# Optimization experiments

Measured on AMD Instinct MI355X. Metric: run time of the kernel, lower is better.

The kernel has to match this reference:

```python
import jax, jax.numpy as jnp
import numpy as np

N = 50000      # num nodes
E = 800000     # num edges (avg degree 16)
H = 128        # hidden_dim
D = 3          # node_dim (decoder output)
L = 4          # num_layers


def setup_inputs() -> dict:
    key = jax.random.key(0)
    ks = jax.random.split(key, 6)
    s = 0.05
    x = jax.random.normal(ks[0], (N, H), dtype=jnp.float32)
    edge_index = jax.random.randint(ks[1], (2, E), 0, N, dtype=jnp.int64)
    # per-layer EdgeConv MLP params: Linear(2H->H), ReLU, Linear(H->H)
    W1 = jax.random.normal(ks[2], (L, 2 * H, H), dtype=jnp.float32) * s
    b1 = jnp.zeros((L, H), dtype=jnp.float32)
    W2 = jax.random.normal(ks[3], (L, H, H), dtype=jnp.float32) * s
    b2 = jnp.zeros((L, H), dtype=jnp.float32)
    # final fc: Linear(H -> D)
    Wf = jax.random.normal(ks[4], (H, D), dtype=jnp.float32) * s
    bf = jnp.zeros((D,), dtype=jnp.float32)
    return {"x": x, "edge_index": edge_index, "W1": W1, "b1": b1,
            "W2": W2, "b2": b2, "Wf": Wf, "bf": bf}


def reference(x, edge_index, W1, b1, W2, b2, Wf, bf):
    n = x.shape[0]
    # add_self_loops: every node has at least one incoming message
    loops = jnp.arange(n, dtype=edge_index.dtype)
    src = jnp.concatenate([edge_index[0], loops])  # x_j source
    dst = jnp.concatenate([edge_index[1], loops])  # x_i target / aggregate index
    for l in range(W1.shape[0]):
        x_i = x[dst]                                   # [E+N, H] gather targets
        x_j = x[src]                                   # [E+N, H] gather sources
        msg = jnp.concatenate([x_i, x_j - x_i], axis=-1)   # [E+N, 2H]
        msg = jax.nn.relu(msg @ W1[l] + b1[l]) @ W2[l] + b2[l]  # edge MLP
        x = jax.ops.segment_max(msg, dst, num_segments=n)       # max aggregate
    return x @ Wf + bf  # [N, D]
```

## Files before the change

### kernel.cpp

```cpp
#include <hip/hip_runtime.h>
#include <hip/hip_fp16.h>

typedef _Float16 f16;
typedef _Float16 f16x8 __attribute__((ext_vector_type(8)));
typedef __fp16 hf16x2 __attribute__((ext_vector_type(2)));
typedef float f32x4 __attribute__((ext_vector_type(4)));
typedef float f32x2 __attribute__((ext_vector_type(2)));

#define HDIM 128
#define LAYERS 4
#define NEG_BIG (-3.0e38f)

static __device__ __forceinline__ f32x4 mfma16(f16x8 a, f16x8 b, f32x4 c) {
  return __builtin_amdgcn_mfma_f32_16x16x32_f16(a, b, c, 0, 0, 0);
}

static __device__ __forceinline__ void atomicMaxF(float* addr, float val) {
  if (val >= 0.f) atomicMax((int*)addr, __float_as_int(val));
  else            atomicMin((unsigned int*)addr, __float_as_uint(val));
}

static __device__ __forceinline__ void split8(f32x4 a, f32x4 b, f16x8& hv, f16x8& lv) {
  hf16x2 h0 = __builtin_amdgcn_cvt_pkrtz(a.x, a.y);
  hf16x2 h1 = __builtin_amdgcn_cvt_pkrtz(a.z, a.w);
  hf16x2 h2 = __builtin_amdgcn_cvt_pkrtz(b.x, b.y);
  hf16x2 h3 = __builtin_amdgcn_cvt_pkrtz(b.z, b.w);
  hv[0]=(f16)h0[0]; hv[1]=(f16)h0[1]; hv[2]=(f16)h1[0]; hv[3]=(f16)h1[1];
  hv[4]=(f16)h2[0]; hv[5]=(f16)h2[1]; hv[6]=(f16)h3[0]; hv[7]=(f16)h3[1];
  hf16x2 l0 = __builtin_amdgcn_cvt_pkrtz(a.x-(float)h0[0], a.y-(float)h0[1]);
  hf16x2 l1 = __builtin_amdgcn_cvt_pkrtz(a.z-(float)h1[0], a.w-(float)h1[1]);
  hf16x2 l2 = __builtin_amdgcn_cvt_pkrtz(b.x-(float)h2[0], b.y-(float)h2[1]);
  hf16x2 l3 = __builtin_amdgcn_cvt_pkrtz(b.z-(float)h3[0], b.w-(float)h3[1]);
  lv[0]=(f16)l0[0]; lv[1]=(f16)l0[1]; lv[2]=(f16)l1[0]; lv[3]=(f16)l1[1];
  lv[4]=(f16)l2[0]; lv[5]=(f16)l2[1]; lv[6]=(f16)l3[0]; lv[7]=(f16)l3[1];
}

__global__ void gnn_hist(const int* __restrict__ ei, int* __restrict__ deg, int E) {
  int e = blockIdx.x * 256 + threadIdx.x;
  if (e < E) atomicAdd(&deg[ei[E + e]], 1);
}

__global__ void gnn_bsum(const int* __restrict__ deg, int* __restrict__ bsum, int N) {
  __shared__ int red[256];
  int v = blockIdx.x * 256 + threadIdx.x;
  red[threadIdx.x] = (v < N) ? (deg[v] + 1) : 0;
  __syncthreads();
  for (int d = 128; d; d >>= 1) {
    if (threadIdx.x < d) red[threadIdx.x] += red[threadIdx.x + d];
    __syncthreads();
  }
  if (threadIdx.x == 0) bsum[blockIdx.x] = red[0];
}

__global__ void gnn_bscan(const int* __restrict__ bsum, int* __restrict__ boffs,
                          int* __restrict__ offs, int nb, int N) {
  __shared__ int sh[256];
  int t = threadIdx.x;
  sh[t] = (t < nb) ? bsum[t] : 0;
  __syncthreads();
  for (int d = 1; d < 256; d <<= 1) {
    int add = (t >= d) ? sh[t - d] : 0;
    __syncthreads();
    sh[t] += add;
    __syncthreads();
  }
  boffs[t] = (t > 0) ? sh[t - 1] : 0;
  if (t == 255) offs[N] = sh[255];
}

__global__ void gnn_scan_fin(const int* __restrict__ deg, const int* __restrict__ boffs,
                             int* __restrict__ offs, int* __restrict__ cursor,
                             int* __restrict__ colsrc, int* __restrict__ nodeof, int N) {
  __shared__ int sh[256];
  int t = threadIdx.x;
  int v = blockIdx.x * 256 + t;
  int val = (v < N) ? (deg[v] + 1) : 0;
  sh[t] = val;
  __syncthreads();
  for (int d = 1; d < 256; d <<= 1) {
    int add = (t >= d) ? sh[t - d] : 0;
    __syncthreads();
    sh[t] += add;
    __syncthreads();
  }
  if (v < N) {
    int excl = boffs[blockIdx.x] + sh[t] - val;
    offs[v] = excl;
    cursor[v] = excl + 1;
    colsrc[excl] = v;
    int e = excl + val;
    for (int s = excl; s < e; s++) nodeof[s] = v;
  }
}

__global__ void gnn_scatter(const int* __restrict__ ei, int* __restrict__ cursor,
                            int* __restrict__ colsrc, int E) {
  int e = blockIdx.x * 256 + threadIdx.x;
  if (e < E) {
    int d = ei[E + e];
    int p = atomicAdd(&cursor[d], 1);
    colsrc[p] = ei[e];
  }
}

__global__ void gnn_biasprep(const float* __restrict__ W1, const float* __restrict__ b1,
                             const float* __restrict__ b2, const float* __restrict__ Wf,
                             const float* __restrict__ bf, float* __restrict__ cbias,
                             float* __restrict__ bfp) {
  int l = blockIdx.x, c = threadIdx.x;
  if (l < LAYERS) {
    float s = 0.f;
    if (l > 0) {
      const float* bp = b2 + (size_t)(l - 1) * HDIM;
      if (c < 128) {
        for (int k = 0; k < 128; k++)
          s += bp[k] * (W1[((size_t)l * 256 + k) * 128 + c] - W1[((size_t)l * 256 + 128 + k) * 128 + c]);
      } else {
        int cc = c - 128;
        for (int k = 0; k < 128; k++)
          s += bp[k] * W1[((size_t)l * 256 + 128 + k) * 128 + cc];
      }
    }
    float base = (c < 128) ? b1[(size_t)l * HDIM + c] : 0.f;
    cbias[l * 256 + c] = base + s;
  } else if (c < 3) {
    float s = bf[c];
    for (int k = 0; k < 128; k++) s += b2[3 * HDIM + k] * Wf[k * 3 + c];
    bfp[c] = s;
  }
}

__global__ void gnn_wprep1(const float* __restrict__ W1, f16* __restrict__ Wc) {
  int id = blockIdx.x * 256 + threadIdx.x;
  if (id >= LAYERS * 128 * 256) return;
  int col = id & 255, k = (id >> 8) & 127, l = id >> 15;
  float w;
  if (col < 128) w = W1[((size_t)l * 256 + k) * 128 + col] - W1[((size_t)l * 256 + 128 + k) * 128 + col];
  else           w = W1[((size_t)l * 256 + 128 + k) * 128 + (col - 128)];
  f16 hi = (f16)w;
  f16 lo = (f16)(w - (float)hi);
  int kk = k >> 5, quad = (k >> 3) & 3, j = k & 7;
  int ntile = col >> 4, lane = quad * 16 + (col & 15);
  size_t base = ((((size_t)l * 2 + 0) * 4 + kk) * 16 + ntile) * 512 + lane * 8 + j;
  Wc[base] = hi;
  Wc[base + (size_t)4 * 16 * 512] = lo;
}

__global__ void gnn_wprep2(const float* __restrict__ W2, f16* __restrict__ W2f) {
  int id = blockIdx.x * 256 + threadIdx.x;
  if (id >= LAYERS * 128 * 128) return;
  int n = id & 127, k = (id >> 7) & 127, l = id >> 14;
  float w = W2[((size_t)l * 128 + k) * 128 + n];
  f16 hi = (f16)w;
  f16 lo = (f16)(w - (float)hi);
  int kk = k >> 5, quad = (k >> 3) & 3, j = k & 7;
  int ntile = n >> 4, lane = quad * 16 + (n & 15);
  size_t base = ((((size_t)l * 2 + 0) * 4 + kk) * 8 + ntile) * 512 + lane * 8 + j;
  W2f[base] = hi;
  W2f[base + (size_t)4 * 8 * 512] = lo;
}

__global__ __launch_bounds__(256) void gnn_pq(const float* __restrict__ x,
    const f16* __restrict__ Wc, const float* __restrict__ cbias,
    float* __restrict__ P, float* __restrict__ Q, int N,
    const int* __restrict__ offs, int spb, float* __restrict__ xinit) {
  __shared__ __align__(16) f16 shA[2 * 4 * 4 * 64 * 8];
  int tid = threadIdx.x;
  int row0 = blockIdx.x * 64;
#pragma unroll
  for (int i = 0; i < 4; i++) {
    int p = i * 256 + tid;
    int row = p & 63, seg = p >> 6;
    f32x4 a = {}, b = {};
    int gr = row0 + row;
    if (gr < N) {
      const f32x4* xp = (const f32x4*)(x + (size_t)gr * HDIM + seg * 8);
      a = xp[0]; b = xp[1];
    }
    f16x8 hv, lv;
    split8(a, b, hv, lv);
    int kk = seg >> 2, quad = seg & 3, mt = row >> 4, m = row & 15;
    int lane = quad * 16 + m;
    int off = ((kk * 4 + mt) * 64 + lane) * 8;
    *(f16x8*)&shA[off] = hv;
    *(f16x8*)&shA[off + 4 * 4 * 64 * 8] = lv;
  }
  __syncthreads();
  int wave = tid >> 6, lane = tid & 63;
  int quad = lane >> 4, cl = lane & 15;
  f16x8 bw[2][4][4];
#pragma unroll
  for (int pl = 0; pl < 2; pl++)
#pragma unroll
    for (int nt = 0; nt < 4; nt++)
#pragma unroll
      for (int kk = 0; kk < 4; kk++) {
        int ntile = wave * 4 + nt;
        bw[pl][nt][kk] = *(const f16x8*)&Wc[(((size_t)(pl * 4 + kk) * 16 + ntile) * 64 + lane) * 8];
      }
#pragma unroll
  for (int mt = 0; mt < 4; mt++) {
    f32x4 acc[4] = {};
#pragma unroll
    for (int kk = 0; kk < 4; kk++) {
      f16x8 ah = *(const f16x8*)&shA[((kk * 4 + mt) * 64 + lane) * 8];
      f16x8 al = *(const f16x8*)&shA[(((4 + kk) * 4 + mt) * 64 + lane) * 8];
#pragma unroll
      for (int nt = 0; nt < 4; nt++) {
        acc[nt] = mfma16(ah, bw[0][nt][kk], acc[nt]);
        acc[nt] = mfma16(al, bw[0][nt][kk], acc[nt]);
        acc[nt] = mfma16(ah, bw[1][nt][kk], acc[nt]);
      }
    }
#pragma unroll
    for (int nt = 0; nt < 4; nt++) {
      int c = (wave * 4 + nt) * 16 + cl;
      float bb = cbias[c];
      float* dst = (c < HDIM) ? P : Q;
      int cc = c & 127;
#pragma unroll
      for (int i = 0; i < 4; i++) {
        int gr = row0 + mt * 16 + quad * 4 + i;
        if (gr < N) dst[(size_t)gr * HDIM + cc] = acc[nt][i] + bb;
      }
    }
  }
  if (tid < 64) {
    int v = row0 + tid;
    if (v < N) {
      int a = offs[v], b = offs[v + 1] - 1;
      if (a / spb != b / spb) {
        f32x4 ninf = {NEG_BIG, NEG_BIG, NEG_BIG, NEG_BIG};
        float* xr = xinit + (size_t)v * HDIM;
#pragma unroll
        for (int c = 0; c < HDIM; c += 4) *(f32x4*)(xr + c) = ninf;
      }
    }
  }
}

__global__ __launch_bounds__(256, 3) void gnn_edge3(
    const float* __restrict__ P, const float* __restrict__ Q,
    const int* __restrict__ offs, const int* __restrict__ colsrc,
    const int* __restrict__ nodeof, const f16* __restrict__ W2f,
    float* __restrict__ xout, int S, int spb) {
  __shared__ __align__(16) f16 shA[2 * 4 * 2 * 64 * 8];
  __shared__ float msg[32 * 132];
  __shared__ float stradV[2][128];
  __shared__ int stradN[2];
  int tid = threadIdx.x;
  int wave = tid >> 6, lane = tid & 63;
  int quad = lane >> 4, cl = lane & 15;
  f16x8 bw[2][2][4];
#pragma unroll
  for (int pl = 0; pl < 2; pl++)
#pragma unroll
    for (int nt = 0; nt < 2; nt++)
#pragma unroll
      for (int kk = 0; kk < 4; kk++)
        bw[pl][nt][kk] = *(const f16x8*)&W2f[(((size_t)(pl * 4 + kk) * 8 + (wave * 2 + nt)) * 64 + lane) * 8];
  int blk0 = blockIdx.x * spb;
  int blk1 = blk0 + spb; if (blk1 > S) blk1 = S;
  if (tid < 2) stradN[tid] = -1;
  int sl = tid >> 4, seg = tid & 15;
  int kkb = seg >> 2, qb = seg & 3;
  int laneF = qb * 16 + sl;
  int tc = 0;
  for (int t0 = blk0; t0 < blk1; t0 += 32, tc++) {
    int par = tc & 1, prv = par ^ 1;
    int tEnd = t0 + 32; if (tEnd > blk1) tEnd = blk1;
#pragma unroll
    for (int i = 0; i < 2; i++) {
      int slot = t0 + i * 16 + sl;
      int slc = (slot < S) ? slot : (S - 1);
      int src = colsrc[slc];
      int dst = nodeof[slc];
      const f32x4* qp = (const f32x4*)(Q + (size_t)src * HDIM + seg * 8);
      const f32x4* pp = (const f32x4*)(P + (size_t)dst * HDIM + seg * 8);
      f32x4 qa = qp[0], qb4 = qp[1], pa = pp[0], pb = pp[1];
      f32x4 sa, sb;
      sa.x = fmaxf(pa.x + qa.x, 0.f); sa.y = fmaxf(pa.y + qa.y, 0.f);
      sa.z = fmaxf(pa.z + qa.z, 0.f); sa.w = fmaxf(pa.w + qa.w, 0.f);
      sb.x = fmaxf(pb.x + qb4.x, 0.f); sb.y = fmaxf(pb.y + qb4.y, 0.f);
      sb.z = fmaxf(pb.z + qb4.z, 0.f); sb.w = fmaxf(pb.w + qb4.w, 0.f);
      f16x8 hv, lv;
      split8(sa, sb, hv, lv);
      int off = ((kkb * 2 + i) * 64 + laneF) * 8;
      *(f16x8*)&shA[off] = hv;
      *(f16x8*)&shA[off + 4096] = lv;
    }
    __syncthreads();
    if (tid == 0) stradN[par] = -1;
    f32x4 acc[2][2] = {};
#pragma unroll
    for (int kk = 0; kk < 4; kk++)
#pragma unroll
      for (int mt = 0; mt < 2; mt++) {
        int off = ((kk * 2 + mt) * 64 + lane) * 8;
        f16x8 ah = *(const f16x8*)&shA[off];
        f16x8 al = *(const f16x8*)&shA[off + 4096];
#pragma unroll
        for (int nt = 0; nt < 2; nt++) {
          acc[mt][nt] = mfma16(ah, bw[0][nt][kk], acc[mt][nt]);
          acc[mt][nt] = mfma16(al, bw[0][nt][kk], acc[mt][nt]);
          acc[mt][nt] = mfma16(ah, bw[1][nt][kk], acc[mt][nt]);
        }
      }
#pragma unroll
    for (int mt = 0; mt < 2; mt++)
#pragma unroll
      for (int nt = 0; nt < 2; nt++) {
        int col = wave * 32 + nt * 16 + cl;
#pragma unroll
        for (int i = 0; i < 4; i++) {
          int row = mt * 16 + quad * 4 + i;
          msg[row * 132 + col] = acc[mt][nt][i];
        }
      }
    __syncthreads();
    int vA = nodeof[t0];
    int vB = nodeof[tEnd - 1];
    int sNp = stradN[prv];
    int npairs = (vB - vA + 1) << 7;
    for (int p = tid; p < npairs; p += 256) {
      int v = vA + (p >> 7), col = p & 127;
      int a = offs[v], b = offs[v + 1];
      int r0 = (a > t0 ? a : t0) - t0;
      int r1 = (b < tEnd ? b : tEnd) - t0;
      float m = NEG_BIG;
      for (int r = r0; r < r1; r++) m = fmaxf(m, msg[r * 132 + col]);
      if (v == sNp) m = fmaxf(m, stradV[prv][col]);
      if (b > tEnd && tEnd < blk1) {
        stradV[par][col] = m;
        if (col == 0) stradN[par] = v;
      } else {
        float* dp = &xout[(size_t)v * HDIM + col];
        if (a < blk0 || b > blk1) atomicMaxF(dp, m);
        else *dp = m;
      }
    }
  }
}

__global__ __launch_bounds__(256) void gnn_fc(const float* __restrict__ x,
    const float* __restrict__ Wf, const float* __restrict__ bfp,
    float* __restrict__ out, int N) {
  int wave = threadIdx.x >> 6, lane = threadIdx.x & 63;
  int wid = blockIdx.x * 4 + wave, nw = gridDim.x * 4;
  int k0 = lane * 2;
  float w00 = Wf[k0 * 3 + 0], w01 = Wf[k0 * 3 + 1], w02 = Wf[k0 * 3 + 2];
  float w10 = Wf[k0 * 3 + 3], w11 = Wf[k0 * 3 + 4], w12 = Wf[k0 * 3 + 5];
  float bf0 = bfp[0], bf1 = bfp[1], bf2 = bfp[2];
  for (int v = wid; v < N; v += nw) {
    f32x2 xx = *(const f32x2*)(x + (size_t)v * HDIM + k0);
    float d0 = xx.x * w00 + xx.y * w10;
    float d1 = xx.x * w01 + xx.y * w11;
    float d2 = xx.x * w02 + xx.y * w12;
#pragma unroll
    for (int s = 32; s; s >>= 1) {
      d0 += __shfl_xor(d0, s, 64);
      d1 += __shfl_xor(d1, s, 64);
      d2 += __shfl_xor(d2, s, 64);
    }
    if (lane == 0) {
      out[(size_t)v * 3 + 0] = d0 + bf0;
      out[(size_t)v * 3 + 1] = d1 + bf1;
      out[(size_t)v * 3 + 2] = d2 + bf2;
    }
  }
}

extern "C" void kernel_launch(void* const* d_in, const int* in_sizes, int n_in,
                              void* d_out, int out_size, void* d_ws, size_t ws_size,
                              hipStream_t stream) {
  const float* x_in = (const float*)d_in[0];
  const int*   ei   = (const int*)d_in[1];
  const float* W1   = (const float*)d_in[2];
  const float* b1   = (const float*)d_in[3];
  const float* W2   = (const float*)d_in[4];
  const float* b2   = (const float*)d_in[5];
  const float* Wf   = (const float*)d_in[6];
  const float* bfv  = (const float*)d_in[7];
  float* outp = (float*)d_out;
  int N = in_sizes[0] / HDIM;
  int E = in_sizes[1] / 2;
  int S = E + N;

  char* ws = (char*)d_ws;
  size_t o = 0;
  auto alloc = [&](size_t bytes) -> char* {
    char* p = ws + o;
    o += (bytes + 255) & ~(size_t)255;
    return p;
  };
  int*   deg    = (int*)alloc((size_t)N * 4);
  int*   offs   = (int*)alloc(((size_t)N + 1) * 4);
  int*   cursor = (int*)alloc((size_t)N * 4);
  int*   colsrc = (int*)alloc((size_t)S * 4);
  int*   nodeof = (int*)alloc((size_t)S * 4);
  int*   bsum   = (int*)alloc(256 * 4);
  int*   boffs  = (int*)alloc(256 * 4);
  float* cbias  = (float*)alloc((size_t)LAYERS * 256 * 4);
  float* bfp    = (float*)alloc(4 * 4);
  float* P      = (float*)alloc((size_t)N * HDIM * 4);
  float* Q      = (float*)alloc((size_t)N * HDIM * 4);
  float* xbuf   = (float*)alloc((size_t)N * HDIM * 4);
  f16*   Wc     = (f16*)alloc((size_t)LAYERS * 65536 * 2);
  f16*   W2f    = (f16*)alloc((size_t)LAYERS * 32768 * 2);
  (void)ws_size; (void)n_in; (void)out_size;

  int nb = (N + 255) / 256;
  hipMemsetAsync(deg, 0, (size_t)N * 4, stream);
  gnn_hist<<<(E + 255) / 256, 256, 0, stream>>>(ei, deg, E);
  gnn_bsum<<<nb, 256, 0, stream>>>(deg, bsum, N);
  gnn_bscan<<<1, 256, 0, stream>>>(bsum, boffs, offs, nb, N);
  gnn_scan_fin<<<nb, 256, 0, stream>>>(deg, boffs, offs, cursor, colsrc, nodeof, N);
  gnn_scatter<<<(E + 255) / 256, 256, 0, stream>>>(ei, cursor, colsrc, E);
  gnn_biasprep<<<LAYERS + 1, 256, 0, stream>>>(W1, b1, b2, Wf, bfv, cbias, bfp);
  gnn_wprep1<<<(LAYERS * 128 * 256 + 255) / 256, 256, 0, stream>>>(W1, Wc);
  gnn_wprep2<<<(LAYERS * 128 * 128 + 255) / 256, 256, 0, stream>>>(W2, W2f);

  int spb = (((S + 1023) / 1024) + 31) & ~31;
  int NB = (S + spb - 1) / spb;
  const float* xc = x_in;
  for (int l = 0; l < LAYERS; l++) {
    gnn_pq<<<(N + 63) / 64, 256, 0, stream>>>(xc, Wc + (size_t)l * 65536, cbias + l * 256,
                                              P, Q, N, offs, spb, xbuf);
    gnn_edge3<<<NB, 256, 0, stream>>>(P, Q, offs, colsrc, nodeof, W2f + (size_t)l * 32768,
                                      xbuf, S, spb);
    xc = xbuf;
  }
  gnn_fc<<<256, 256, 0, stream>>>(xc, Wf, bfp, outp, N);
}
```

Measured before the change: 867.5 us.

## Enlarge edge tile to 48 rows and vectorize segment-max reduction

Raises the edge tile in the fused edge MLP kernel from 32 to 48 slots, so each barrier and weight-register pass covers more MFMA work, and aligns the per-block slot span to the new tile size. The segment-max reduction now has each thread handle four columns with f32x4 shared-memory loads and vector global stores instead of one column per thread. The f16 hi/lo split packs converted pairs via bitcast instead of element-wise assignment. The larger tile raises shared-memory use and accumulator registers, which may lower occupancy under the 3-blocks launch bound.

After: 926.7 us. 6.8% more time.

```diff
diff --git a/kernel.cpp b/kernel.cpp
--- a/kernel.cpp
+++ b/kernel.cpp
@@ -6,9 +6,12 @@
 typedef __fp16 hf16x2 __attribute__((ext_vector_type(2)));
 typedef float f32x4 __attribute__((ext_vector_type(4)));
 typedef float f32x2 __attribute__((ext_vector_type(2)));
+typedef unsigned int u32;
+typedef u32 u32x4 __attribute__((ext_vector_type(4)));
 
 #define HDIM 128
 #define LAYERS 4
+#define TS 48
 #define NEG_BIG (-3.0e38f)
 
 static __device__ __forceinline__ f32x4 mfma16(f16x8 a, f16x8 b, f32x4 c) {
@@ -18,6 +21,12 @@
 static __device__ __forceinline__ void atomicMaxF(float* addr, float val) {
   if (val >= 0.f) atomicMax((int*)addr, __float_as_int(val));
   else            atomicMin((unsigned int*)addr, __float_as_uint(val));
+}
+
+static __device__ __forceinline__ f16x8 pack4(hf16x2 a, hf16x2 b, hf16x2 c, hf16x2 d) {
+  u32x4 u = {__builtin_bit_cast(u32, a), __builtin_bit_cast(u32, b),
+             __builtin_bit_cast(u32, c), __builtin_bit_cast(u32, d)};
+  return __builtin_bit_cast(f16x8, u);
 }
 
 static __device__ __forceinline__ void split8(f32x4 a, f32x4 b, f16x8& hv, f16x8& lv) {
@@ -25,14 +34,12 @@
   hf16x2 h1 = __builtin_amdgcn_cvt_pkrtz(a.z, a.w);
   hf16x2 h2 = __builtin_amdgcn_cvt_pkrtz(b.x, b.y);
   hf16x2 h3 = __builtin_amdgcn_cvt_pkrtz(b.z, b.w);
-  hv[0]=(f16)h0[0]; hv[1]=(f16)h0[1]; hv[2]=(f16)h1[0]; hv[3]=(f16)h1[1];
-  hv[4]=(f16)h2[0]; hv[5]=(f16)h2[1]; hv[6]=(f16)h3[0]; hv[7]=(f16)h3[1];
-  hf16x2 l0 = __builtin_amdgcn_cvt_pkrtz(a.x-(float)h0[0], a.y-(float)h0[1]);
-  hf16x2 l1 = __builtin_amdgcn_cvt_pkrtz(a.z-(float)h1[0], a.w-(float)h1[1]);
-  hf16x2 l2 = __builtin_amdgcn_cvt_pkrtz(b.x-(float)h2[0], b.y-(float)h2[1]);
-  hf16x2 l3 = __builtin_amdgcn_cvt_pkrtz(b.z-(float)h3[0], b.w-(float)h3[1]);
-  lv[0]=(f16)l0[0]; lv[1]=(f16)l0[1]; lv[2]=(f16)l1[0]; lv[3]=(f16)l1[1];
-  lv[4]=(f16)l2[0]; lv[5]=(f16)l2[1]; lv[6]=(f16)l3[0]; lv[7]=(f16)l3[1];
+  hv = pack4(h0, h1, h2, h3);
+  hf16x2 l0 = __builtin_amdgcn_cvt_pkrtz(a.x - (float)h0[0], a.y - (float)h0[1]);
+  hf16x2 l1 = __builtin_amdgcn_cvt_pkrtz(a.z - (float)h1[0], a.w - (float)h1[1]);
+  hf16x2 l2 = __builtin_amdgcn_cvt_pkrtz(b.x - (float)h2[0], b.y - (float)h2[1]);
+  hf16x2 l3 = __builtin_amdgcn_cvt_pkrtz(b.z - (float)h3[0], b.w - (float)h3[1]);
+  lv = pack4(l0, l1, l2, l3);
 }
 
 __global__ void gnn_hist(const int* __restrict__ ei, int* __restrict__ deg, int E) {
@@ -239,14 +246,14 @@
   }
 }
 
-__global__ __launch_bounds__(256, 3) void gnn_edge3(
+__global__ __launch_bounds__(256, 3) void gnn_edge4(
     const float* __restrict__ P, const float* __restrict__ Q,
     const int* __restrict__ offs, const int* __restrict__ colsrc,
     const int* __restrict__ nodeof, const f16* __restrict__ W2f,
     float* __restrict__ xout, int S, int spb) {
-  __shared__ __align__(16) f16 shA[2 * 4 * 2 * 64 * 8];
-  __shared__ float msg[32 * 132];
-  __shared__ float stradV[2][128];
+  __shared__ __align__(16) f16 shA[2 * 4 * 3 * 64 * 8];
+  __shared__ __align__(16) float msg[TS * 132];
+  __shared__ __align__(16) float stradV[2][128];
   __shared__ int stradN[2];
   int tid = threadIdx.x;
   int wave = tid >> 6, lane = tid & 63;
@@ -266,11 +273,11 @@
   int kkb = seg >> 2, qb = seg & 3;
   int laneF = qb * 16 + sl;
   int tc = 0;
-  for (int t0 = blk0; t0 < blk1; t0 += 32, tc++) {
+  for (int t0 = blk0; t0 < blk1; t0 += TS, tc++) {
     int par = tc & 1, prv = par ^ 1;
-    int tEnd = t0 + 32; if (tEnd > blk1) tEnd = blk1;
-#pragma unroll
-    for (int i = 0; i < 2; i++) {
+    int tEnd = t0 + TS; if (tEnd > blk1) tEnd = blk1;
+#pragma unroll
+    for (int i = 0; i < 3; i++) {
       int slot = t0 + i * 16 + sl;
       int slc = (slot < S) ? slot : (S - 1);
       int src = colsrc[slc];
@@ -285,20 +292,20 @@
       sb.z = fmaxf(pb.z + qb4.z, 0.f); sb.w = fmaxf(pb.w + qb4.w, 0.f);
       f16x8 hv, lv;
       split8(sa, sb, hv, lv);
-      int off = ((kkb * 2 + i) * 64 + laneF) * 8;
+      int off = ((kkb * 3 + i) * 64 + laneF) * 8;
       *(f16x8*)&shA[off] = hv;
-      *(f16x8*)&shA[off + 4096] = lv;
+      *(f16x8*)&shA[off + 6144] = lv;
     }
     __syncthreads();
     if (tid == 0) stradN[par] = -1;
-    f32x4 acc[2][2] = {};
+    f32x4 acc[3][2] = {};
 #pragma unroll
     for (int kk = 0; kk < 4; kk++)
 #pragma unroll
-      for (int mt = 0; mt < 2; mt++) {
-        int off = ((kk * 2 + mt) * 64 + lane) * 8;
+      for (int mt = 0; mt < 3; mt++) {
+        int off = ((kk * 3 + mt) * 64 + lane) * 8;
         f16x8 ah = *(const f16x8*)&shA[off];
-        f16x8 al = *(const f16x8*)&shA[off + 4096];
+        f16x8 al = *(const f16x8*)&shA[off + 6144];
 #pragma unroll
         for (int nt = 0; nt < 2; nt++) {
           acc[mt][nt] = mfma16(ah, bw[0][nt][kk], acc[mt][nt]);
@@ -307,7 +314,7 @@
         }
       }
 #pragma unroll
-    for (int mt = 0; mt < 2; mt++)
+    for (int mt = 0; mt < 3; mt++)
 #pragma unroll
       for (int nt = 0; nt < 2; nt++) {
         int col = wave * 32 + nt * 16 + cl;
@@ -321,22 +328,34 @@
     int vA = nodeof[t0];
     int vB = nodeof[tEnd - 1];
     int sNp = stradN[prv];
-    int npairs = (vB - vA + 1) << 7;
-    for (int p = tid; p < npairs; p += 256) {
-      int v = vA + (p >> 7), col = p & 127;
+    int ngroups = (vB - vA + 1) << 5;
+    for (int p = tid; p < ngroups; p += 256) {
+      int v = vA + (p >> 5), c4 = (p & 31) << 2;
       int a = offs[v], b = offs[v + 1];
       int r0 = (a > t0 ? a : t0) - t0;
       int r1 = (b < tEnd ? b : tEnd) - t0;
-      float m = NEG_BIG;
-      for (int r = r0; r < r1; r++) m = fmaxf(m, msg[r * 132 + col]);
-      if (v == sNp) m = fmaxf(m, stradV[prv][col]);
+      f32x4 m = {NEG_BIG, NEG_BIG, NEG_BIG, NEG_BIG};
+      for (int r = r0; r < r1; r++) {
+        f32x4 x = *(const f32x4*)&msg[r * 132 + c4];
+        m.x = fmaxf(m.x, x.x); m.y = fmaxf(m.y, x.y);
+        m.z = fmaxf(m.z, x.z); m.w = fmaxf(m.w, x.w);
+      }
+      if (v == sNp) {
+        f32x4 sv = *(const f32x4*)&stradV[prv][c4];
+        m.x = fmaxf(m.x, sv.x); m.y = fmaxf(m.y, sv.y);
+        m.z = fmaxf(m.z, sv.z); m.w = fmaxf(m.w, sv.w);
+      }
       if (b > tEnd && tEnd < blk1) {
-        stradV[par][col] = m;
-        if (col == 0) stradN[par] = v;
+        *(f32x4*)&stradV[par][c4] = m;
+        if ((p & 31) == 0) stradN[par] = v;
       } else {
-        float* dp = &xout[(size_t)v * HDIM + col];
-        if (a < blk0 || b > blk1) atomicMaxF(dp, m);
-        else *dp = m;
+        float* dp = &xout[(size_t)v * HDIM + c4];
+        if (a < blk0 || b > blk1) {
+          atomicMaxF(dp + 0, m.x); atomicMaxF(dp + 1, m.y);
+          atomicMaxF(dp + 2, m.z); atomicMaxF(dp + 3, m.w);
+        } else {
+          *(f32x4*)dp = m;
+        }
       }
     }
   }
@@ -420,13 +439,13 @@
   gnn_wprep1<<<(LAYERS * 128 * 256 + 255) / 256, 256, 0, stream>>>(W1, Wc);
   gnn_wprep2<<<(LAYERS * 128 * 128 + 255) / 256, 256, 0, stream>>>(W2, W2f);
 
-  int spb = (((S + 1023) / 1024) + 31) & ~31;
+  int spb = ((((S + 1023) / 1024) + TS - 1) / TS) * TS;
   int NB = (S + spb - 1) / spb;
   const float* xc = x_in;
   for (int l = 0; l < LAYERS; l++) {
     gnn_pq<<<(N + 63) / 64, 256, 0, stream>>>(xc, Wc + (size_t)l * 65536, cbias + l * 256,
                                               P, Q, N, offs, spb, xbuf);
-    gnn_edge3<<<NB, 256, 0, stream>>>(P, Q, offs, colsrc, nodeof, W2f + (size_t)l * 32768,
+    gnn_edge4<<<NB, 256, 0, stream>>>(P, Q, offs, colsrc, nodeof, W2f + (size_t)l * 32768,
                                       xbuf, S, spb);
     xc = xbuf;
   }
```
